# Optimization experiments

Measured on AMD Instinct MI355X. Metric: run time of the kernel, lower is better.

The kernel has to match this reference:

```python
import jax, jax.numpy as jnp
import numpy as np


def setup_inputs() -> dict:
    key = jax.random.key(0)
    ks = jax.random.split(key, 9)
    B, T, I, H = 4096, 512, 10, 32
    return {
        "x": jax.random.normal(ks[0], (B, T, I), dtype=jnp.float32),
        "h0": jax.random.normal(ks[1], (B, H), dtype=jnp.float32),
        "c0": jax.random.normal(ks[2], (B, H), dtype=jnp.float32),
        "W_ih": jax.random.normal(ks[3], (4 * H, I), dtype=jnp.float32) * 0.1,
        "W_hh": jax.random.normal(ks[4], (4 * H, H), dtype=jnp.float32) * 0.1,
        "b_ih": jax.random.normal(ks[5], (4 * H,), dtype=jnp.float32) * 0.1,
        "b_hh": jax.random.normal(ks[6], (4 * H,), dtype=jnp.float32) * 0.1,
        "W_lin": jax.random.normal(ks[7], (1, H), dtype=jnp.float32) * 0.1,
        "b_lin": jax.random.normal(ks[8], (1,), dtype=jnp.float32) * 0.1,
    }


def _lstm_final_hidden(x, h0, c0, W_ih, W_hh, b_ih, b_hh):
    H = h0.shape[-1]
    # Precompute input contribution for all timesteps: [B,T,4H]
    x_gates = jnp.einsum("bti,gi->btg", x, W_ih) + b_ih + b_hh
    x_gates_t = jnp.swapaxes(x_gates, 0, 1)  # [T,B,4H] for scan

    def step(carry, xg):
        h, c = carry
        gates = xg + h @ W_hh.T  # [B,4H]
        i = jax.nn.sigmoid(gates[:, 0 * H:1 * H])
        f = jax.nn.sigmoid(gates[:, 1 * H:2 * H])
        g = jnp.tanh(gates[:, 2 * H:3 * H])
        o = jax.nn.sigmoid(gates[:, 3 * H:4 * H])
        c_new = f * c + i * g
        h_new = o * jnp.tanh(c_new)
        return (h_new, c_new), None

    (hT, cT), _ = jax.lax.scan(step, (h0, c0), x_gates_t)
    return hT


def reference(x, h0, c0, W_ih, W_hh, b_ih, b_hh, W_lin, b_lin):
    hT = _lstm_final_hidden(x, h0, c0, W_ih, W_hh, b_ih, b_hh)  # [B,H]
    return hT @ W_lin.T + b_lin  # [B,1]
```

## Files before the change

### kernel.cpp

```cpp
#include <hip/hip_runtime.h>

#define TT 512
#define II 10
#define HH 32
#define LOG2E 1.44269504088896340736f

typedef __attribute__((ext_vector_type(8))) short bf16x8;
typedef __attribute__((ext_vector_type(4))) float f32x4;
typedef __attribute__((ext_vector_type(4))) int   i32x4;

#define MFMA(A, B, C) __builtin_amdgcn_mfma_f32_16x16x32_bf16((A), (B), (C), 0, 0, 0)

static __device__ __forceinline__ float frcp(float v) { return __builtin_amdgcn_rcpf(v); }
static __device__ __forceinline__ float fexp2(float v) { return __builtin_amdgcn_exp2f(v); }

static __device__ __forceinline__ short bf16rne(float f) {
    unsigned u = __builtin_bit_cast(unsigned, f);
    u += 0x7fffu + ((u >> 16) & 1u);
    return (short)(u >> 16);
}
static __device__ __forceinline__ unsigned pk2(float a, float b) {
    return __builtin_amdgcn_perm(__builtin_bit_cast(unsigned, b),
                                 __builtin_bit_cast(unsigned, a), 0x07060302u);
}
static __device__ __forceinline__ unsigned pkh(float a, float b) {
    return __builtin_amdgcn_perm(__builtin_bit_cast(unsigned, b) + 0x8000u,
                                 __builtin_bit_cast(unsigned, a) + 0x8000u, 0x07060302u);
}

extern "C" __global__ __launch_bounds__(256)
__attribute__((amdgpu_waves_per_eu(1)))
void lstm_mfma(const float* __restrict__ x,
               const float* __restrict__ h0,
               const float* __restrict__ c0,
               const float* __restrict__ W_ih,
               const float* __restrict__ W_hh,
               const float* __restrict__ b_ih,
               const float* __restrict__ b_hh,
               const float* __restrict__ W_lin,
               const float* __restrict__ b_lin,
               float* __restrict__ out)
{
    __shared__ int   hx[2][4][16][4];
    __shared__ float plds[64];

    const int tid  = threadIdx.x;
    const int w    = tid >> 6;
    const int lane = tid & 63;
    const int n    = lane & 15;
    const int q    = lane >> 4;
    const int R    = blockIdx.x * 16;

    const int   gate = n & 3;
    const float sc   = (gate == 2) ? 2.0f * LOG2E : LOG2E;
    bf16x8 AhA, AhB, AxA, AxB;
    #pragma unroll
    for (int st = 0; st < 2; ++st) {
        const int s     = 2 * w + st;
        const int unitm = 4 * s + (n >> 2);
        const int Wr    = gate * HH + unitm;
        bf16x8 ah, ax;
        #pragma unroll
        for (int j = 0; j < 8; ++j) {
            ah[j] = bf16rne(W_hh[Wr * HH + 4 * j + q] * sc);
            const int k = q * 8 + j;
            float xv = 0.0f;
            if (k < II)       xv = W_ih[Wr * II + k] * sc;
            else if (k == II) xv = (b_ih[Wr] + b_hh[Wr]) * sc;
            ax[j] = bf16rne(xv);
        }
        if (st == 0) { AhA = ah; AxA = ax; } else { AhB = ah; AxB = ax; }
    }

    const int uA = 8 * w + q, uB = uA + 4;
    float cA = c0[(R + n) * HH + uA];
    float cB = c0[(R + n) * HH + uB];
    const float wlA = W_lin[uA], wlB = W_lin[uB];

    hx[0][w][n][q] = (int)pkh(h0[(R + n) * HH + uA], h0[(R + n) * HH + uB]);
    __syncthreads();

    const float* xp = x + (size_t)(R + n) * (TT * II);
    float2 xl0 = *(const float2*)(xp + 0), xl1 = *(const float2*)(xp + 2),
           xl2 = *(const float2*)(xp + 4), xl3 = *(const float2*)(xp + 6),
           xl4 = *(const float2*)(xp + 8);

    const bool q0 = (q == 0), q1 = (q == 1);
    const f32x4 z4 = {0.0f, 0.0f, 0.0f, 0.0f};
    float hA = 0.0f, hB = 0.0f;

    for (int t = 0; t < TT; ++t) {
        const int rb = t & 1;
        const int b0 = hx[rb][0][n][q];
        const int b1 = hx[rb][1][n][q];
        const int b2 = hx[rb][2][n][q];
        const int b3 = hx[rb][3][n][q];

        const unsigned d0 = q0 ? pk2(xl0.x, xl0.y) : (q1 ? pk2(xl4.x, xl4.y) : 0u);
        const unsigned d1 = q0 ? pk2(xl1.x, xl1.y) : (q1 ? 0x00003F80u : 0u);
        const unsigned d2 = q0 ? pk2(xl2.x, xl2.y) : 0u;
        const unsigned d3 = q0 ? pk2(xl3.x, xl3.y) : 0u;
        const bf16x8 Bx = __builtin_bit_cast(bf16x8, (i32x4){(int)d0, (int)d1, (int)d2, (int)d3});

        f32x4 accA = MFMA(AxA, Bx, z4);
        f32x4 accB = MFMA(AxB, Bx, z4);

        {
            const float* px = xp + (size_t)((t + 1 < TT) ? t + 1 : t) * II;
            xl0 = *(const float2*)(px + 0); xl1 = *(const float2*)(px + 2);
            xl2 = *(const float2*)(px + 4); xl3 = *(const float2*)(px + 6);
            xl4 = *(const float2*)(px + 8);
        }

        const bf16x8 Bh = __builtin_bit_cast(bf16x8, (i32x4){b0, b1, b2, b3});
        accA = MFMA(AhA, Bh, accA);
        accB = MFMA(AhB, Bh, accB);

        {
            const float ri = frcp(1.0f + fexp2(-accA[0]));
            const float rf = frcp(1.0f + fexp2(-accA[1]));
            const float rg = frcp(1.0f + fexp2(-accA[2]));
            const float ro = frcp(1.0f + fexp2(-accA[3]));
            cA = rf * cA + ri * (2.0f * rg - 1.0f);
            const float rt = frcp(1.0f + fexp2(cA * (-2.0f * LOG2E)));
            hA = ro * (2.0f * rt - 1.0f);
        }
        {
            const float ri = frcp(1.0f + fexp2(-accB[0]));
            const float rf = frcp(1.0f + fexp2(-accB[1]));
            const float rg = frcp(1.0f + fexp2(-accB[2]));
            const float ro = frcp(1.0f + fexp2(-accB[3]));
            cB = rf * cB + ri * (2.0f * rg - 1.0f);
            const float rt = frcp(1.0f + fexp2(cB * (-2.0f * LOG2E)));
            hB = ro * (2.0f * rt - 1.0f);
        }
        hx[1 - rb][w][n][q] = (int)pkh(hA, hB);
        __syncthreads();
    }

    float p = hA * wlA + hB * wlB;
    p += __shfl_xor(p, 16);
    p += __shfl_xor(p, 32);
    if (q == 0) plds[w * 16 + n] = p;
    __syncthreads();
    if (tid < 16) {
        out[R + tid] = plds[tid] + plds[16 + tid] + plds[32 + tid] + plds[48 + tid] + b_lin[0];
    }
}

extern "C" void kernel_launch(void* const* d_in, const int* in_sizes, int n_in,
                              void* d_out, int out_size, void* d_ws, size_t ws_size,
                              hipStream_t stream) {
    const float* x     = (const float*)d_in[0];
    const float* h0    = (const float*)d_in[1];
    const float* c0    = (const float*)d_in[2];
    const float* W_ih  = (const float*)d_in[3];
    const float* W_hh  = (const float*)d_in[4];
    const float* b_ih  = (const float*)d_in[5];
    const float* b_hh  = (const float*)d_in[6];
    const float* W_lin = (const float*)d_in[7];
    const float* b_lin = (const float*)d_in[8];
    float* out = (float*)d_out;

    const int B = in_sizes[1] / HH;
    dim3 grid(B / 16), block(256);
    lstm_mfma<<<grid, block, 0, stream>>>(x, h0, c0, W_ih, W_hh, b_ih, b_hh, W_lin, b_lin, out);
}
```

Before: 350.8 us.

## Run each LSTM batch tile in one wave with register-resident hidden state

Each 16-row batch tile now runs in a single 64-lane wave that computes all 32 hidden units: eight gate tiles per step instead of two per wave across four waves. The recurrent hidden state is packed straight into the MFMA B operand in registers. This removes the per-timestep LDS exchange and block-wide barrier. The time loop is also unrolled by two with double-buffered x prefetch. The trade-off is four times more MFMA and transcendental work per wave, all on one SIMD per block, and more register pressure.

Measured after the change: 549.0 us. 1.56x slower.

```diff
diff --git a/kernel.cpp b/kernel.cpp
--- a/kernel.cpp
+++ b/kernel.cpp
@@ -28,7 +28,7 @@
                                  __builtin_bit_cast(unsigned, a) + 0x8000u, 0x07060302u);
 }
 
-extern "C" __global__ __launch_bounds__(256)
+extern "C" __global__ __launch_bounds__(64)
 __attribute__((amdgpu_waves_per_eu(1)))
 void lstm_mfma(const float* __restrict__ x,
                const float* __restrict__ h0,
@@ -41,111 +41,102 @@
                const float* __restrict__ b_lin,
                float* __restrict__ out)
 {
-    __shared__ int   hx[2][4][16][4];
-    __shared__ float plds[64];
-
-    const int tid  = threadIdx.x;
-    const int w    = tid >> 6;
-    const int lane = tid & 63;
+    const int lane = threadIdx.x & 63;
     const int n    = lane & 15;
     const int q    = lane >> 4;
     const int R    = blockIdx.x * 16;
 
     const int   gate = n & 3;
     const float sc   = (gate == 2) ? 2.0f * LOG2E : LOG2E;
-    bf16x8 AhA, AhB, AxA, AxB;
+
+    bf16x8 Ah[8], Ax[8];
+    float  c[8], wl[8], h[8];
     #pragma unroll
-    for (int st = 0; st < 2; ++st) {
-        const int s     = 2 * w + st;
+    for (int s = 0; s < 8; ++s) {
         const int unitm = 4 * s + (n >> 2);
         const int Wr    = gate * HH + unitm;
-        bf16x8 ah, ax;
         #pragma unroll
         for (int j = 0; j < 8; ++j) {
-            ah[j] = bf16rne(W_hh[Wr * HH + 4 * j + q] * sc);
+            Ah[s][j] = bf16rne(W_hh[Wr * HH + 4 * j + q] * sc);
             const int k = q * 8 + j;
             float xv = 0.0f;
             if (k < II)       xv = W_ih[Wr * II + k] * sc;
             else if (k == II) xv = (b_ih[Wr] + b_hh[Wr]) * sc;
-            ax[j] = bf16rne(xv);
+            Ax[s][j] = bf16rne(xv);
         }
-        if (st == 0) { AhA = ah; AxA = ax; } else { AhB = ah; AxB = ax; }
+        const int u = 4 * s + q;
+        c[s]  = c0[(R + n) * HH + u];
+        wl[s] = W_lin[u];
     }
 
-    const int uA = 8 * w + q, uB = uA + 4;
-    float cA = c0[(R + n) * HH + uA];
-    float cB = c0[(R + n) * HH + uB];
-    const float wlA = W_lin[uA], wlB = W_lin[uB];
-
-    hx[0][w][n][q] = (int)pkh(h0[(R + n) * HH + uA], h0[(R + n) * HH + uB]);
-    __syncthreads();
+    i32x4 Bh;
+    #pragma unroll
+    for (int d = 0; d < 4; ++d)
+        Bh[d] = (int)pkh(h0[(R + n) * HH + 8 * d + q],
+                         h0[(R + n) * HH + 8 * d + 4 + q]);
 
     const float* xp = x + (size_t)(R + n) * (TT * II);
-    float2 xl0 = *(const float2*)(xp + 0), xl1 = *(const float2*)(xp + 2),
-           xl2 = *(const float2*)(xp + 4), xl3 = *(const float2*)(xp + 6),
-           xl4 = *(const float2*)(xp + 8);
+    float2 e0 = *(const float2*)(xp + 0), e1 = *(const float2*)(xp + 2),
+           e2 = *(const float2*)(xp + 4), e3 = *(const float2*)(xp + 6),
+           e4 = *(const float2*)(xp + 8);
+    float2 o0 = *(const float2*)(xp + II + 0), o1 = *(const float2*)(xp + II + 2),
+           o2 = *(const float2*)(xp + II + 4), o3 = *(const float2*)(xp + II + 6),
+           o4 = *(const float2*)(xp + II + 8);
 
     const bool q0 = (q == 0), q1 = (q == 1);
     const f32x4 z4 = {0.0f, 0.0f, 0.0f, 0.0f};
-    float hA = 0.0f, hB = 0.0f;
 
-    for (int t = 0; t < TT; ++t) {
-        const int rb = t & 1;
-        const int b0 = hx[rb][0][n][q];
-        const int b1 = hx[rb][1][n][q];
-        const int b2 = hx[rb][2][n][q];
-        const int b3 = hx[rb][3][n][q];
-
-        const unsigned d0 = q0 ? pk2(xl0.x, xl0.y) : (q1 ? pk2(xl4.x, xl4.y) : 0u);
-        const unsigned d1 = q0 ? pk2(xl1.x, xl1.y) : (q1 ? 0x00003F80u : 0u);
-        const unsigned d2 = q0 ? pk2(xl2.x, xl2.y) : 0u;
-        const unsigned d3 = q0 ? pk2(xl3.x, xl3.y) : 0u;
+    auto STEP = [&](float2& l0, float2& l1, float2& l2, float2& l3, float2& l4,
+                    int pf) {
+        const unsigned d0 = q0 ? pk2(l0.x, l0.y) : (q1 ? pk2(l4.x, l4.y) : 0u);
+        const unsigned d1 = q0 ? pk2(l1.x, l1.y) : (q1 ? 0x00003F80u : 0u);
+        const unsigned d2 = q0 ? pk2(l2.x, l2.y) : 0u;
+        const unsigned d3 = q0 ? pk2(l3.x, l3.y) : 0u;
         const bf16x8 Bx = __builtin_bit_cast(bf16x8, (i32x4){(int)d0, (int)d1, (int)d2, (int)d3});
 
-        f32x4 accA = MFMA(AxA, Bx, z4);
-        f32x4 accB = MFMA(AxB, Bx, z4);
+        f32x4 acc[8];
+        #pragma unroll
+        for (int s = 0; s < 8; ++s) acc[s] = MFMA(Ax[s], Bx, z4);
 
         {
-            const float* px = xp + (size_t)((t + 1 < TT) ? t + 1 : t) * II;
-            xl0 = *(const float2*)(px + 0); xl1 = *(const float2*)(px + 2);
-            xl2 = *(const float2*)(px + 4); xl3 = *(const float2*)(px + 6);
-            xl4 = *(const float2*)(px + 8);
+            const float* px = xp + (size_t)pf * II;
+            l0 = *(const float2*)(px + 0); l1 = *(const float2*)(px + 2);
+            l2 = *(const float2*)(px + 4); l3 = *(const float2*)(px + 6);
+            l4 = *(const float2*)(px + 8);
         }
 
-        const bf16x8 Bh = __builtin_bit_cast(bf16x8, (i32x4){b0, b1, b2, b3});
-        accA = MFMA(AhA, Bh, accA);
-        accB = MFMA(AhB, Bh, accB);
+        const bf16x8 BhF = __builtin_bit_cast(bf16x8, Bh);
+        #pragma unroll
+        for (int s = 0; s < 8; ++s) acc[s] = MFMA(Ah[s], BhF, acc[s]);
 
-        {
-            const float ri = frcp(1.0f + fexp2(-accA[0]));
-            const float rf = frcp(1.0f + fexp2(-accA[1]));
-            const float rg = frcp(1.0f + fexp2(-accA[2]));
-            const float ro = frcp(1.0f + fexp2(-accA[3]));
-            cA = rf * cA + ri * (2.0f * rg - 1.0f);
-            const float rt = frcp(1.0f + fexp2(cA * (-2.0f * LOG2E)));
-            hA = ro * (2.0f * rt - 1.0f);
+        #pragma unroll
+        for (int s = 0; s < 8; ++s) {
+            const float ri = frcp(1.0f + fexp2(-acc[s][0]));
+            const float rf = frcp(1.0f + fexp2(-acc[s][1]));
+            const float rg = frcp(1.0f + fexp2(-acc[s][2]));
+            const float ro = frcp(1.0f + fexp2(-acc[s][3]));
+            c[s] = rf * c[s] + ri * (2.0f * rg - 1.0f);
+            const float rt = frcp(1.0f + fexp2(c[s] * (-2.0f * LOG2E)));
+            h[s] = ro * (2.0f * rt - 1.0f);
         }
-        {
-            const float ri = frcp(1.0f + fexp2(-accB[0]));
-            const float rf = frcp(1.0f + fexp2(-accB[1]));
-            const float rg = frcp(1.0f + fexp2(-accB[2]));
-            const float ro = frcp(1.0f + fexp2(-accB[3]));
-            cB = rf * cB + ri * (2.0f * rg - 1.0f);
-            const float rt = frcp(1.0f + fexp2(cB * (-2.0f * LOG2E)));
-            hB = ro * (2.0f * rt - 1.0f);
-        }
-        hx[1 - rb][w][n][q] = (int)pkh(hA, hB);
-        __syncthreads();
+        #pragma unroll
+        for (int d = 0; d < 4; ++d) Bh[d] = (int)pkh(h[2 * d], h[2 * d + 1]);
+    };
+
+    #pragma unroll 1
+    for (int t = 0; t < TT; t += 2) {
+        const int pfe = (t + 2 < TT) ? t + 2 : TT - 1;
+        const int pfo = (t + 3 < TT) ? t + 3 : TT - 1;
+        STEP(e0, e1, e2, e3, e4, pfe);
+        STEP(o0, o1, o2, o3, o4, pfo);
     }
 
-    float p = hA * wlA + hB * wlB;
+    float p = 0.0f;
+    #pragma unroll
+    for (int s = 0; s < 8; ++s) p += h[s] * wl[s];
     p += __shfl_xor(p, 16);
     p += __shfl_xor(p, 32);
-    if (q == 0) plds[w * 16 + n] = p;
-    __syncthreads();
-    if (tid < 16) {
-        out[R + tid] = plds[tid] + plds[16 + tid] + plds[32 + tid] + plds[48 + tid] + b_lin[0];
-    }
+    if (lane < 16) out[R + lane] = p + b_lin[0];
 }
 
 extern "C" void kernel_launch(void* const* d_in, const int* in_sizes, int n_in,
@@ -163,6 +154,6 @@
     float* out = (float*)d_out;
 
     const int B = in_sizes[1] / HH;
-    dim3 grid(B / 16), block(256);
+    dim3 grid(B / 16), block(64);
     lstm_mfma<<<grid, block, 0, stream>>>(x, h0, c0, W_ih, W_hh, b_ih, b_hh, W_lin, b_lin, out);
 }
```
